# Optimization experiments

Hardware: AMD Instinct MI355X
Metric: run time of the kernel (lower is better)

Reference implementation:

```python
import jax, jax.numpy as jnp
import numpy as np

N_CHANNELS = 512
GROUPS = 8
EPS = 1e-5


def setup_inputs() -> dict:
    key = jax.random.key(0)
    ks = jax.random.split(key, 7)
    B, C, L = 8, N_CHANNELS, 4096
    s = 1.0 / np.sqrt(C)
    return {
        "x": jax.random.normal(ks[0], (B, C, L), dtype=jnp.float32),
        "gamma": jnp.ones((C,), dtype=jnp.float32),
        "beta": jnp.zeros((C,), dtype=jnp.float32),
        "w_qkv": jax.random.normal(ks[1], (3 * C, C), dtype=jnp.float32) * s,
        "b_qkv": jax.random.normal(ks[2], (3 * C,), dtype=jnp.float32) * 0.01,
        "w_out": jax.random.normal(ks[3], (C, C), dtype=jnp.float32) * s,
        "b_out": jax.random.normal(ks[4], (C,), dtype=jnp.float32) * 0.01,
    }


def group_norm(x, gamma, beta):
    # x: [B, C, L]; normalize per group of C//GROUPS channels over (channels_in_group, L)
    B, C, L = x.shape
    xg = x.reshape(B, GROUPS, C // GROUPS, L)
    mean = xg.mean(axis=(2, 3), keepdims=True)
    var = xg.var(axis=(2, 3), keepdims=True)
    xn = ((xg - mean) * jax.lax.rsqrt(var + EPS)).reshape(B, C, L)
    return xn * gamma[None, :, None] + beta[None, :, None]


def reference(x, gamma, beta, w_qkv, b_qkv, w_out, b_out):
    B, C, L = x.shape
    xn = group_norm(x, gamma, beta)
    # 1x1 conv == channel matmul: [3C, C] @ [B, C, L] -> [B, 3C, L]
    qkv = jnp.einsum('oc,bcl->bol', w_qkv, xn) + b_qkv[None, :, None]
    q, k, v = jnp.split(qkv, 3, axis=1)  # each [B, C, L]
    scale = C ** (-0.5)
    attn = jnp.einsum('bcl,bck->blk', q, k) * scale  # [B, L, L]
    attn = jax.nn.softmax(attn, axis=-1)
    out = jnp.einsum('blk,bck->bcl', attn, v)  # [B, C, L]
    proj = jnp.einsum('oc,bcl->bol', w_out, out) + b_out[None, :, None]
    return x + proj
```

## Files before the change

### kernel.cpp

```cpp
#include <hip/hip_runtime.h>

typedef __attribute__((ext_vector_type(4))) float f32x4;
typedef __attribute__((ext_vector_type(8))) short short8;
typedef unsigned short u16;
typedef unsigned int u32;

static constexpr int Bb = 8, Cc = 512, Ll = 4096;

__device__ __forceinline__ u16 f2bf(float f) {
  u32 u = __builtin_bit_cast(u32, f);
  u = (u + 0x7FFFu + ((u >> 16) & 1u)) >> 16;
  return (u16)u;
}

__device__ __forceinline__ void load_lds16(const void* g, void* l) {
  __builtin_amdgcn_global_load_lds((const __attribute__((address_space(1))) void*)g,
                                   (__attribute__((address_space(3))) void*)l,
                                   16, 0, 0);
}

__global__ void cvt_bf16_kernel(const float* __restrict__ src, u16* __restrict__ dst, int n) {
  int stride = gridDim.x * blockDim.x;
  for (int i = blockIdx.x * blockDim.x + threadIdx.x; i < n; i += stride)
    dst[i] = f2bf(src[i]);
}

__global__ __launch_bounds__(256)
void gn_stats_kernel(const float* __restrict__ x, float* __restrict__ stats) {
  int bg = blockIdx.x;
  const f32x4* p = (const f32x4*)(x + (size_t)bg * (64 * Ll));
  float s = 0.f, ss = 0.f;
  for (int i = threadIdx.x; i < 64 * Ll / 4; i += 256) {
    f32x4 v = p[i];
    s  += v[0] + v[1] + v[2] + v[3];
    ss += v[0]*v[0] + v[1]*v[1] + v[2]*v[2] + v[3]*v[3];
  }
  __shared__ float rs[256], rq[256];
  rs[threadIdx.x] = s; rq[threadIdx.x] = ss;
  __syncthreads();
  for (int st = 128; st > 0; st >>= 1) {
    if (threadIdx.x < st) { rs[threadIdx.x] += rs[threadIdx.x + st]; rq[threadIdx.x] += rq[threadIdx.x + st]; }
    __syncthreads();
  }
  if (threadIdx.x == 0) {
    const float inv_n = 1.f / (64.f * 4096.f);
    float mean = rs[0] * inv_n;
    float var  = rq[0] * inv_n - mean * mean;
    stats[bg * 2]     = mean;
    stats[bg * 2 + 1] = rsqrtf(var + 1e-5f);
  }
}

__global__ __launch_bounds__(256)
void gn_apply_t_kernel(const float* __restrict__ x, const float* __restrict__ gamma,
                       const float* __restrict__ beta, const float* __restrict__ stats,
                       u16* __restrict__ xn_t) {
  int lt = blockIdx.x;
  int ct = blockIdx.y;
  int b  = blockIdx.z;
  __shared__ float tile[64][65];
  int t = threadIdx.x;
  int lx = t & 63;
  int qd = t >> 6;
  int c0 = ct * 64, l0 = lt * 64;
  float mean = stats[(b * 8 + ct) * 2];
  float rstd = stats[(b * 8 + ct) * 2 + 1];
  #pragma unroll
  for (int i = 0; i < 16; ++i) {
    int cl = qd + i * 4;
    int c = c0 + cl;
    float v = x[((size_t)b * Cc + c) * Ll + l0 + lx];
    tile[cl][lx] = (v - mean) * rstd * gamma[c] + beta[c];
  }
  __syncthreads();
  #pragma unroll
  for (int i = 0; i < 16; ++i) {
    int ll = qd + i * 4;
    xn_t[((size_t)b * Ll + l0 + ll) * Cc + c0 + lx] = f2bf(tile[lx][ll]);
  }
}

template <int MODE>
__global__ __launch_bounds__(256, 2)
void gemm_tn(const u16* __restrict__ A, long long aStride, int lda,
             const u16* __restrict__ Bm, long long bStride, int ldb,
             void* __restrict__ Dv, long long dStride, int ldd,
             const float* __restrict__ bias, const float* __restrict__ resid, int K) {
  int z = blockIdx.z;
  A  += (size_t)z * aStride;
  Bm += (size_t)z * bStride;
  int m0 = blockIdx.x * 128, n0 = blockIdx.y * 128;
  __shared__ uint4 sA[1024], sB[1024];
  int tid = threadIdx.x, lane = tid & 63;
  int wv = tid >> 6, wr = wv >> 1, wc = wv & 1;
  int l15 = lane & 15, l4 = lane >> 4;
  f32x4 acc[4][4] = {};
  for (int kt = 0; kt < K; kt += 64) {
    __syncthreads();
    #pragma unroll
    for (int p = 0; p < 4; ++p) {
      int s = p * 256 + tid;
      int r = ((s >> 7) << 4) | (((s >> 2) & 1) << 3) | ((s >> 3) & 7);
      int g = (((s >> 6) & 1) << 2) | (s & 3);
      load_lds16(A  + (size_t)(m0 + r) * lda + kt + g * 8, &sA[s]);
      load_lds16(Bm + (size_t)(n0 + r) * ldb + kt + g * 8, &sB[s]);
    }
    __syncthreads();
    #pragma unroll
    for (int ks = 0; ks < 2; ++ks) {
      short8 af[4], bfr[4];
      #pragma unroll
      for (int i = 0; i < 4; ++i) {
        int sa = (4 * wr + i) * 128 + ks * 64 + (l15 & 7) * 8 + (l15 >> 3) * 4 + l4;
        af[i]  = *(const short8*)&sA[sa];
        int sb = (4 * wc + i) * 128 + ks * 64 + (l15 & 7) * 8 + (l15 >> 3) * 4 + l4;
        bfr[i] = *(const short8*)&sB[sb];
      }
      #pragma unroll
      for (int i = 0; i < 4; ++i)
        #pragma unroll
        for (int j = 0; j < 4; ++j)
          acc[i][j] = __builtin_amdgcn_mfma_f32_16x16x32_bf16(af[i], bfr[j], acc[i][j], 0, 0, 0);
    }
  }
  #pragma unroll
  for (int i = 0; i < 4; ++i) {
    #pragma unroll
    for (int j = 0; j < 4; ++j) {
      #pragma unroll
      for (int r = 0; r < 4; ++r) {
        int m = m0 + 64 * wr + 16 * i + 4 * l4 + r;
        int n = n0 + 64 * wc + 16 * j + l15;
        float val = acc[i][j][r] + (MODE == 0 ? bias[n] : bias[m]);
        size_t idx = (size_t)z * dStride + (size_t)m * ldd + n;
        if (MODE == 2) ((float*)Dv)[idx] = val + resid[idx];
        else           ((u16*)Dv)[idx]   = f2bf(val);
      }
    }
  }
}

__global__ __launch_bounds__(512, 2)
void flash_attn_kernel(const u16* __restrict__ qk_t, const u16* __restrict__ v,
                       u16* __restrict__ o_t) {
  int bid = blockIdx.x;
  int b  = bid & 7;
  int q0 = (bid >> 3) * 128;
  int tid = threadIdx.x, lane = tid & 63, wv = tid >> 6;
  int l15 = lane & 15, l4 = lane >> 4;
  const u16* qkb = qk_t + (size_t)b * Ll * 1024;
  const u16* vb  = v    + (size_t)b * Cc * Ll;
  u16* ob        = o_t  + (size_t)b * Ll * Cc;

  __shared__ uint4 sK[2][32 * 64];
  __shared__ uint4 sV[2][512 * 4];
  __shared__ __align__(16) char sP[128 * 64];
  __shared__ __align__(16) float sAl[128];

  int ow_q = wv >> 2, ow_c = wv & 3;

  short8 aq[16];
  {
    const u16* qp = qkb + (size_t)(q0 + wv * 16 + l15) * 1024 + 8 * l4;
    #pragma unroll
    for (int ks = 0; ks < 16; ++ks) aq[ks] = *(const short8*)(qp + 32 * ks);
  }

  auto issueK = [&](int kt, int buf) {
    #pragma unroll
    for (int p = 0; p < 4; ++p) {
      int s = p * 512 + tid;
      int kr = (((s >> 6) & 1) << 4) | (((s >> 2) & 1) << 3) | ((s >> 3) & 7);
      int g  = ((s >> 7) << 2) | (s & 3);
      load_lds16(qkb + (size_t)(kt * 32 + kr) * 1024 + 512 + g * 8, &sK[buf][s]);
    }
  };
  auto issueV = [&](int kt, int buf) {
    #pragma unroll
    for (int p = 0; p < 4; ++p) {
      int s = p * 512 + tid;
      int r = s >> 2, g = s & 3, gw = g ^ ((r >> 1) & 3);
      load_lds16(vb + (size_t)r * Ll + kt * 32 + gw * 8, &sV[buf][s]);
    }
  };
  issueK(0, 0);
  issueV(0, 0);

  f32x4 accO[4][8];
  #pragma unroll
  for (int i = 0; i < 4; ++i)
    #pragma unroll
    for (int j = 0; j < 8; ++j) accO[i][j] = (f32x4){0.f, 0.f, 0.f, 0.f};
  float mrun = -1e30f, lrun = 0.f;
  const float scale = 0.044194173824159216f;

  const int NT = Ll / 32;
  for (int kt = 0; kt < NT; ++kt) {
    int buf = kt & 1;
    __syncthreads();
    if (kt + 1 < NT) { issueK(kt + 1, buf ^ 1); issueV(kt + 1, buf ^ 1); }

    const uint4* kb = &sK[buf][0];
    f32x4 s2[2];
    #pragma unroll
    for (int t = 0; t < 2; ++t) {
      s2[t] = (f32x4){0.f, 0.f, 0.f, 0.f};
      #pragma unroll
      for (int ks = 0; ks < 16; ++ks) {
        short8 ak = *(const short8*)&kb[ks * 128 + t * 64 + (l15 & 7) * 8 + (l15 >> 3) * 4 + l4];
        s2[t] = __builtin_amdgcn_mfma_f32_16x16x32_bf16(ak, aq[ks], s2[t], 0, 0, 0);
      }
    }

    #pragma unroll
    for (int t = 0; t < 2; ++t)
      #pragma unroll
      for (int r = 0; r < 4; ++r) s2[t][r] *= scale;
    float mx = fmaxf(fmaxf(s2[0][0], s2[0][1]), fmaxf(s2[0][2], s2[0][3]));
    mx = fmaxf(mx, fmaxf(fmaxf(s2[1][0], s2[1][1]), fmaxf(s2[1][2], s2[1][3])));
    mx = fmaxf(mx, __shfl_xor(mx, 16));
    mx = fmaxf(mx, __shfl_xor(mx, 32));
    float mnew = fmaxf(mrun, mx);
    float al = __expf(mrun - mnew);
    mrun = mnew;
    float ps = 0.f;
    #pragma unroll
    for (int t = 0; t < 2; ++t)
      #pragma unroll
      for (int r = 0; r < 4; ++r) { float pv = __expf(s2[t][r] - mnew); s2[t][r] = pv; ps += pv; }
    ps += __shfl_xor(ps, 16);
    ps += __shfl_xor(ps, 32);
    lrun = lrun * al + ps;

    {
      char* pb = sP + (16 * wv + l15) * 64;
      #pragma unroll
      for (int t = 0; t < 2; ++t) {
        u32 lo = (u32)f2bf(s2[t][0]) | ((u32)f2bf(s2[t][1]) << 16);
        u32 hi = (u32)f2bf(s2[t][2]) | ((u32)f2bf(s2[t][3]) << 16);
        uint2 w = {lo, hi};
        *(uint2*)(pb + 32 * t + 8 * l4) = w;
      }
      if (lane < 16) sAl[16 * wv + lane] = al;
    }

    __builtin_amdgcn_sched_barrier(0);
    asm volatile("s_waitcnt lgkmcnt(0)" ::: "memory");
    __builtin_amdgcn_s_barrier();
    __builtin_amdgcn_sched_barrier(0);

    #pragma unroll
    for (int i = 0; i < 4; ++i) {
      f32x4 av = *(const f32x4*)&sAl[64 * ow_q + 16 * i + 4 * l4];
      #pragma unroll
      for (int j = 0; j < 8; ++j) {
        #pragma unroll
        for (int r = 0; r < 4; ++r) accO[i][j][r] *= av[r];
      }
    }
    short8 ap[4];
    #pragma unroll
    for (int i = 0; i < 4; ++i) {
      int ra = 64 * ow_q + 16 * i + l15;
      ap[i] = *(const short8*)(sP + ra * 64 + 16 * l4);
    }
    const uint4* vbuf = &sV[buf][0];
    #pragma unroll
    for (int j = 0; j < 8; ++j) {
      int crow = 128 * ow_c + 16 * j + l15;
      short8 bv = *(const short8*)&vbuf[crow * 4 + (l4 ^ ((crow >> 1) & 3))];
      #pragma unroll
      for (int i = 0; i < 4; ++i)
        accO[i][j] = __builtin_amdgcn_mfma_f32_16x16x32_bf16(ap[i], bv, accO[i][j], 0, 0, 0);
    }
  }

  __syncthreads();
  if (lane < 16) sAl[16 * wv + lane] = lrun;
  __syncthreads();
  #pragma unroll
  for (int i = 0; i < 4; ++i) {
    f32x4 lv = *(const f32x4*)&sAl[64 * ow_q + 16 * i + 4 * l4];
    #pragma unroll
    for (int r = 0; r < 4; ++r) lv[r] = 1.f / lv[r];
    #pragma unroll
    for (int j = 0; j < 8; ++j) {
      #pragma unroll
      for (int r = 0; r < 4; ++r) {
        int q = q0 + 64 * ow_q + 16 * i + 4 * l4 + r;
        int c = 128 * ow_c + 16 * j + l15;
        ob[(size_t)q * Cc + c] = f2bf(accO[i][j][r] * lv[r]);
      }
    }
  }
}

extern "C" void kernel_launch(void* const* d_in, const int* in_sizes, int n_in,
                              void* d_out, int out_size, void* d_ws, size_t ws_size,
                              hipStream_t stream) {
  const float* x     = (const float*)d_in[0];
  const float* gamma = (const float*)d_in[1];
  const float* beta  = (const float*)d_in[2];
  const float* w_qkv = (const float*)d_in[3];
  const float* b_qkv = (const float*)d_in[4];
  const float* w_out = (const float*)d_in[5];
  const float* b_out = (const float*)d_in[6];
  float* out = (float*)d_out;

  char* ws = (char*)d_ws;
  size_t off = 0;
  auto alloc = [&](size_t bytes) -> char* {
    char* p = ws + off;
    off += (bytes + 1023) & ~(size_t)1023;
    return p;
  };
  float* stats = (float*)alloc(64 * 2 * sizeof(float));
  u16* wqb = (u16*)alloc((size_t)1536 * 512 * 2);
  u16* wob = (u16*)alloc((size_t)512 * 512 * 2);
  u16* xnt = (u16*)alloc((size_t)Bb * Ll * Cc * 2);
  u16* qkt = (u16*)alloc((size_t)Bb * Ll * 1024 * 2);
  u16* vbf = (u16*)alloc((size_t)Bb * Cc * Ll * 2);
  u16* ot  = xnt;
  if (off > ws_size) return;

  cvt_bf16_kernel<<<256, 256, 0, stream>>>(w_qkv, wqb, 1536 * 512);
  cvt_bf16_kernel<<<256, 256, 0, stream>>>(w_out, wob, 512 * 512);
  gn_stats_kernel<<<64, 256, 0, stream>>>(x, stats);
  gn_apply_t_kernel<<<dim3(64, 8, 8), 256, 0, stream>>>(x, gamma, beta, stats, xnt);
  gemm_tn<0><<<dim3(32, 8, 8), 256, 0, stream>>>(
      xnt, (long long)Ll * Cc, Cc, wqb, 0, Cc,
      qkt, (long long)Ll * 1024, 1024, b_qkv, nullptr, Cc);
  gemm_tn<1><<<dim3(4, 32, 8), 256, 0, stream>>>(
      wqb + (size_t)1024 * 512, 0, Cc, xnt, (long long)Ll * Cc, Cc,
      vbf, (long long)Cc * Ll, Ll, b_qkv + 1024, nullptr, Cc);
  flash_attn_kernel<<<256, 512, 0, stream>>>(qkt, vbf, ot);
  gemm_tn<2><<<dim3(4, 32, 8), 256, 0, stream>>>(
      wob, 0, Cc, ot, (long long)Ll * Cc, Cc,
      out, (long long)Cc * Ll, Ll, b_out, x, Cc);
}
```

Measured before the change: 684.6 us.

## Software-pipeline flash attention so QK of next tile overlaps PV of previous

Restructures the attention loop so each iteration computes QK^T and softmax for tile kt while doing the rescale and PV MFMAs for tile kt-1. P and the rescale factors are double-buffered in LDS, which removes the second barrier per iteration. V loads are issued one stage later than K loads. The change also switches the K LDS layout to an XOR swizzle and pads P rows to 112 bytes to cut bank conflicts. The cost is more LDS and a more complex prologue and epilogue.

```diff
diff --git a/kernel.cpp b/kernel.cpp
--- a/kernel.cpp
+++ b/kernel.cpp
@@ -154,25 +154,17 @@
 
   __shared__ uint4 sK[2][32 * 64];
   __shared__ uint4 sV[2][512 * 4];
-  __shared__ __align__(16) char sP[128 * 64];
-  __shared__ __align__(16) float sAl[128];
+  __shared__ __align__(16) char sP[2][128 * 112];
+  __shared__ __align__(16) float sAl[2][128];
 
   int ow_q = wv >> 2, ow_c = wv & 3;
-
-  short8 aq[16];
-  {
-    const u16* qp = qkb + (size_t)(q0 + wv * 16 + l15) * 1024 + 8 * l4;
-    #pragma unroll
-    for (int ks = 0; ks < 16; ++ks) aq[ks] = *(const short8*)(qp + 32 * ks);
-  }
 
   auto issueK = [&](int kt, int buf) {
     #pragma unroll
     for (int p = 0; p < 4; ++p) {
       int s = p * 512 + tid;
-      int kr = (((s >> 6) & 1) << 4) | (((s >> 2) & 1) << 3) | ((s >> 3) & 7);
-      int g  = ((s >> 7) << 2) | (s & 3);
-      load_lds16(qkb + (size_t)(kt * 32 + kr) * 1024 + 512 + g * 8, &sK[buf][s]);
+      int r = s >> 6, g = s & 63, gw = g ^ (r & 7);
+      load_lds16(qkb + (size_t)(kt * 32 + r) * 1024 + 512 + gw * 8, &sK[buf][s]);
     }
   };
   auto issueV = [&](int kt, int buf) {
@@ -183,8 +175,15 @@
       load_lds16(vb + (size_t)r * Ll + kt * 32 + gw * 8, &sV[buf][s]);
     }
   };
+
   issueK(0, 0);
-  issueV(0, 0);
+
+  short8 aq[16];
+  {
+    const u16* qp = qkb + (size_t)(q0 + wv * 16 + l15) * 1024 + 8 * l4;
+    #pragma unroll
+    for (int ks = 0; ks < 16; ++ks) aq[ks] = *(const short8*)(qp + 32 * ks);
+  }
 
   f32x4 accO[4][8];
   #pragma unroll
@@ -193,25 +192,22 @@
     for (int j = 0; j < 8; ++j) accO[i][j] = (f32x4){0.f, 0.f, 0.f, 0.f};
   float mrun = -1e30f, lrun = 0.f;
   const float scale = 0.044194173824159216f;
-
   const int NT = Ll / 32;
-  for (int kt = 0; kt < NT; ++kt) {
-    int buf = kt & 1;
-    __syncthreads();
-    if (kt + 1 < NT) { issueK(kt + 1, buf ^ 1); issueV(kt + 1, buf ^ 1); }
-
+
+  auto qk_compute = [&](int buf, f32x4* s2) {
     const uint4* kb = &sK[buf][0];
-    f32x4 s2[2];
     #pragma unroll
     for (int t = 0; t < 2; ++t) {
       s2[t] = (f32x4){0.f, 0.f, 0.f, 0.f};
+      int krow = 16 * t + l15;
       #pragma unroll
       for (int ks = 0; ks < 16; ++ks) {
-        short8 ak = *(const short8*)&kb[ks * 128 + t * 64 + (l15 & 7) * 8 + (l15 >> 3) * 4 + l4];
+        short8 ak = *(const short8*)&kb[krow * 64 + ((4 * ks + l4) ^ (krow & 7))];
         s2[t] = __builtin_amdgcn_mfma_f32_16x16x32_bf16(ak, aq[ks], s2[t], 0, 0, 0);
       }
     }
-
+  };
+  auto softmax_store = [&](int buf, f32x4* s2) {
     #pragma unroll
     for (int t = 0; t < 2; ++t)
       #pragma unroll
@@ -231,27 +227,20 @@
     ps += __shfl_xor(ps, 16);
     ps += __shfl_xor(ps, 32);
     lrun = lrun * al + ps;
-
-    {
-      char* pb = sP + (16 * wv + l15) * 64;
-      #pragma unroll
-      for (int t = 0; t < 2; ++t) {
-        u32 lo = (u32)f2bf(s2[t][0]) | ((u32)f2bf(s2[t][1]) << 16);
-        u32 hi = (u32)f2bf(s2[t][2]) | ((u32)f2bf(s2[t][3]) << 16);
-        uint2 w = {lo, hi};
-        *(uint2*)(pb + 32 * t + 8 * l4) = w;
-      }
-      if (lane < 16) sAl[16 * wv + lane] = al;
-    }
-
-    __builtin_amdgcn_sched_barrier(0);
-    asm volatile("s_waitcnt lgkmcnt(0)" ::: "memory");
-    __builtin_amdgcn_s_barrier();
-    __builtin_amdgcn_sched_barrier(0);
-
+    char* pb = &sP[buf][0] + (16 * wv + l15) * 112;
+    #pragma unroll
+    for (int t = 0; t < 2; ++t) {
+      u32 lo = (u32)f2bf(s2[t][0]) | ((u32)f2bf(s2[t][1]) << 16);
+      u32 hi = (u32)f2bf(s2[t][2]) | ((u32)f2bf(s2[t][3]) << 16);
+      uint2 w = {lo, hi};
+      *(uint2*)(pb + 32 * t + 8 * l4) = w;
+    }
+    if (lane < 16) sAl[buf][16 * wv + lane] = al;
+  };
+  auto rescale_pv = [&](int pb) {
     #pragma unroll
     for (int i = 0; i < 4; ++i) {
-      f32x4 av = *(const f32x4*)&sAl[64 * ow_q + 16 * i + 4 * l4];
+      f32x4 av = *(const f32x4*)&sAl[pb][64 * ow_q + 16 * i + 4 * l4];
       #pragma unroll
       for (int j = 0; j < 8; ++j) {
         #pragma unroll
@@ -262,9 +251,9 @@
     #pragma unroll
     for (int i = 0; i < 4; ++i) {
       int ra = 64 * ow_q + 16 * i + l15;
-      ap[i] = *(const short8*)(sP + ra * 64 + 16 * l4);
-    }
-    const uint4* vbuf = &sV[buf][0];
+      ap[i] = *(const short8*)(&sP[pb][0] + ra * 112 + 16 * l4);
+    }
+    const uint4* vbuf = &sV[pb][0];
     #pragma unroll
     for (int j = 0; j < 8; ++j) {
       int crow = 128 * ow_c + 16 * j + l15;
@@ -273,14 +262,35 @@
       for (int i = 0; i < 4; ++i)
         accO[i][j] = __builtin_amdgcn_mfma_f32_16x16x32_bf16(ap[i], bv, accO[i][j], 0, 0, 0);
     }
-  }
-
-  __syncthreads();
-  if (lane < 16) sAl[16 * wv + lane] = lrun;
+  };
+
+  __syncthreads();
+  issueK(1, 1);
+  issueV(0, 0);
+  {
+    f32x4 s2[2];
+    qk_compute(0, s2);
+    softmax_store(0, s2);
+  }
+
+  for (int kt = 1; kt < NT; ++kt) {
+    int buf = kt & 1;
+    __syncthreads();
+    if (kt + 1 < NT) issueK(kt + 1, buf ^ 1);
+    issueV(kt, buf);
+    f32x4 s2[2];
+    qk_compute(buf, s2);
+    rescale_pv(buf ^ 1);
+    softmax_store(buf, s2);
+  }
+
+  __syncthreads();
+  rescale_pv((NT - 1) & 1);
+  if (lane < 16) sAl[NT & 1][16 * wv + lane] = lrun;
   __syncthreads();
   #pragma unroll
   for (int i = 0; i < 4; ++i) {
-    f32x4 lv = *(const f32x4*)&sAl[64 * ow_q + 16 * i + 4 * l4];
+    f32x4 lv = *(const f32x4*)&sAl[NT & 1][64 * ow_q + 16 * i + 4 * l4];
     #pragma unroll
     for (int r = 0; r < 4; ++r) lv[r] = 1.f / lv[r];
     #pragma unroll
```

After: 736.6 us. 7.6% more time.

## Shrink attention blocks to 64 queries with single-buffered swizzled K/V tiles

Applied to the files above, without the earlier changes.

The flash attention kernel now uses 256-thread blocks handling 64 queries each, doubling the grid to 512 blocks. The K/V double-buffer prefetch is replaced by a single buffer loaded each iteration, with a partial vmcnt wait so the QK product can start once K has arrived while V is still loading. K tiles use a row-XOR swizzle and the P buffer rows are padded to reduce LDS bank conflicts. This aims to improve occupancy and load balance, but it doubles K/V global traffic per query and exposes load latency that was previously hidden by prefetching.

```diff
diff --git a/kernel.cpp b/kernel.cpp
--- a/kernel.cpp
+++ b/kernel.cpp
@@ -140,24 +140,22 @@
   }
 }
 
-__global__ __launch_bounds__(512, 2)
+__global__ __launch_bounds__(256, 2)
 void flash_attn_kernel(const u16* __restrict__ qk_t, const u16* __restrict__ v,
                        u16* __restrict__ o_t) {
   int bid = blockIdx.x;
   int b  = bid & 7;
-  int q0 = (bid >> 3) * 128;
+  int q0 = (bid >> 3) * 64;
   int tid = threadIdx.x, lane = tid & 63, wv = tid >> 6;
   int l15 = lane & 15, l4 = lane >> 4;
   const u16* qkb = qk_t + (size_t)b * Ll * 1024;
   const u16* vb  = v    + (size_t)b * Cc * Ll;
   u16* ob        = o_t  + (size_t)b * Ll * Cc;
 
-  __shared__ uint4 sK[2][32 * 64];
-  __shared__ uint4 sV[2][512 * 4];
-  __shared__ __align__(16) char sP[128 * 64];
-  __shared__ __align__(16) float sAl[128];
-
-  int ow_q = wv >> 2, ow_c = wv & 3;
+  __shared__ uint4 sK[32 * 64];
+  __shared__ uint4 sV[512 * 4];
+  __shared__ __align__(16) char sP[64 * 80];
+  __shared__ __align__(16) float sAl[64];
 
   short8 aq[16];
   {
@@ -166,25 +164,22 @@
     for (int ks = 0; ks < 16; ++ks) aq[ks] = *(const short8*)(qp + 32 * ks);
   }
 
-  auto issueK = [&](int kt, int buf) {
-    #pragma unroll
-    for (int p = 0; p < 4; ++p) {
-      int s = p * 512 + tid;
-      int kr = (((s >> 6) & 1) << 4) | (((s >> 2) & 1) << 3) | ((s >> 3) & 7);
-      int g  = ((s >> 7) << 2) | (s & 3);
-      load_lds16(qkb + (size_t)(kt * 32 + kr) * 1024 + 512 + g * 8, &sK[buf][s]);
+  auto issueK = [&](int kt) {
+    #pragma unroll
+    for (int p = 0; p < 8; ++p) {
+      int s = p * 256 + tid;
+      int r = s >> 6, g = s & 63, gw = g ^ (r & 7);
+      load_lds16(qkb + (size_t)(kt * 32 + r) * 1024 + 512 + gw * 8, &sK[s]);
     }
   };
-  auto issueV = [&](int kt, int buf) {
-    #pragma unroll
-    for (int p = 0; p < 4; ++p) {
-      int s = p * 512 + tid;
+  auto issueV = [&](int kt) {
+    #pragma unroll
+    for (int p = 0; p < 8; ++p) {
+      int s = p * 256 + tid;
       int r = s >> 2, g = s & 3, gw = g ^ ((r >> 1) & 3);
-      load_lds16(vb + (size_t)r * Ll + kt * 32 + gw * 8, &sV[buf][s]);
+      load_lds16(vb + (size_t)r * Ll + kt * 32 + gw * 8, &sV[s]);
     }
   };
-  issueK(0, 0);
-  issueV(0, 0);
 
   f32x4 accO[4][8];
   #pragma unroll
@@ -196,18 +191,21 @@
 
   const int NT = Ll / 32;
   for (int kt = 0; kt < NT; ++kt) {
-    int buf = kt & 1;
     __syncthreads();
-    if (kt + 1 < NT) { issueK(kt + 1, buf ^ 1); issueV(kt + 1, buf ^ 1); }
-
-    const uint4* kb = &sK[buf][0];
+    issueK(kt);
+    issueV(kt);
+    asm volatile("s_waitcnt vmcnt(8)" ::: "memory");
+    __builtin_amdgcn_s_barrier();
+    __builtin_amdgcn_sched_barrier(0);
+
     f32x4 s2[2];
     #pragma unroll
     for (int t = 0; t < 2; ++t) {
       s2[t] = (f32x4){0.f, 0.f, 0.f, 0.f};
+      int krow = 16 * t + l15;
       #pragma unroll
       for (int ks = 0; ks < 16; ++ks) {
-        short8 ak = *(const short8*)&kb[ks * 128 + t * 64 + (l15 & 7) * 8 + (l15 >> 3) * 4 + l4];
+        short8 ak = *(const short8*)&sK[krow * 64 + ((4 * ks + l4) ^ (krow & 7))];
         s2[t] = __builtin_amdgcn_mfma_f32_16x16x32_bf16(ak, aq[ks], s2[t], 0, 0, 0);
       }
     }
@@ -233,7 +231,7 @@
     lrun = lrun * al + ps;
 
     {
-      char* pb = sP + (16 * wv + l15) * 64;
+      char* pb = sP + (16 * wv + l15) * 80;
       #pragma unroll
       for (int t = 0; t < 2; ++t) {
         u32 lo = (u32)f2bf(s2[t][0]) | ((u32)f2bf(s2[t][1]) << 16);
@@ -245,13 +243,13 @@
     }
 
     __builtin_amdgcn_sched_barrier(0);
-    asm volatile("s_waitcnt lgkmcnt(0)" ::: "memory");
+    asm volatile("s_waitcnt vmcnt(0) lgkmcnt(0)" ::: "memory");
     __builtin_amdgcn_s_barrier();
     __builtin_amdgcn_sched_barrier(0);
 
     #pragma unroll
     for (int i = 0; i < 4; ++i) {
-      f32x4 av = *(const f32x4*)&sAl[64 * ow_q + 16 * i + 4 * l4];
+      f32x4 av = *(const f32x4*)&sAl[16 * i + 4 * l4];
       #pragma unroll
       for (int j = 0; j < 8; ++j) {
         #pragma unroll
@@ -261,14 +259,13 @@
     short8 ap[4];
     #pragma unroll
     for (int i = 0; i < 4; ++i) {
-      int ra = 64 * ow_q + 16 * i + l15;
-      ap[i] = *(const short8*)(sP + ra * 64 + 16 * l4);
-    }
-    const uint4* vbuf = &sV[buf][0];
+      int ra = 16 * i + l15;
+      ap[i] = *(const short8*)(sP + ra * 80 + 16 * l4);
+    }
     #pragma unroll
     for (int j = 0; j < 8; ++j) {
-      int crow = 128 * ow_c + 16 * j + l15;
-      short8 bv = *(const short8*)&vbuf[crow * 4 + (l4 ^ ((crow >> 1) & 3))];
+      int crow = 128 * wv + 16 * j + l15;
+      short8 bv = *(const short8*)&sV[crow * 4 + (l4 ^ ((crow >> 1) & 3))];
       #pragma unroll
       for (int i = 0; i < 4; ++i)
         accO[i][j] = __builtin_amdgcn_mfma_f32_16x16x32_bf16(ap[i], bv, accO[i][j], 0, 0, 0);
@@ -280,15 +277,15 @@
   __syncthreads();
   #pragma unroll
   for (int i = 0; i < 4; ++i) {
-    f32x4 lv = *(const f32x4*)&sAl[64 * ow_q + 16 * i + 4 * l4];
+    f32x4 lv = *(const f32x4*)&sAl[16 * i + 4 * l4];
     #pragma unroll
     for (int r = 0; r < 4; ++r) lv[r] = 1.f / lv[r];
     #pragma unroll
     for (int j = 0; j < 8; ++j) {
       #pragma unroll
       for (int r = 0; r < 4; ++r) {
-        int q = q0 + 64 * ow_q + 16 * i + 4 * l4 + r;
-        int c = 128 * ow_c + 16 * j + l15;
+        int q = q0 + 16 * i + 4 * l4 + r;
+        int c = 128 * wv + 16 * j + l15;
         ob[(size_t)q * Cc + c] = f2bf(accO[i][j][r] * lv[r]);
       }
     }
@@ -333,7 +330,7 @@
   gemm_tn<1><<<dim3(4, 32, 8), 256, 0, stream>>>(
       wqb + (size_t)1024 * 512, 0, Cc, xnt, (long long)Ll * Cc, Cc,
       vbf, (long long)Cc * Ll, Ll, b_qkv + 1024, nullptr, Cc);
-  flash_attn_kernel<<<256, 512, 0, stream>>>(qkt, vbf, ot);
+  flash_attn_kernel<<<512, 256, 0, stream>>>(qkt, vbf, ot);
   gemm_tn<2><<<dim3(4, 32, 8), 256, 0, stream>>>(
       wob, 0, Cc, ot, (long long)Ll * Cc, Cc,
       out, (long long)Cc * Ll, Ll, b_out, x, Cc);
```

New measurement: 841.0 us. +22.8%, slower.

## Use 64-key tiles with single-buffered K/V and staggered async loads

Applied to the files above, without the earlier changes.

Doubles the key tile per iteration from 32 to 64 and halves the loop trip count. K and V move from double-buffered LDS to single buffers with an XOR swizzle. The next K tile is issued once the QK^T phase is done, and the next V tile after the PV phase, with vmcnt waits in between. The aim is fewer barriers and softmax-rescale passes per key, keeping LDS use near 150KB for two blocks per CU, but load latency is now overlapped with only half of each iteration's compute.

```diff
diff --git a/kernel.cpp b/kernel.cpp
--- a/kernel.cpp
+++ b/kernel.cpp
@@ -152,9 +152,9 @@
   const u16* vb  = v    + (size_t)b * Cc * Ll;
   u16* ob        = o_t  + (size_t)b * Ll * Cc;
 
-  __shared__ uint4 sK[2][32 * 64];
-  __shared__ uint4 sV[2][512 * 4];
-  __shared__ __align__(16) char sP[128 * 64];
+  __shared__ uint4 sK[64 * 64];
+  __shared__ uint4 sV[512 * 8];
+  __shared__ __align__(16) char sP[128 * 144];
   __shared__ __align__(16) float sAl[128];
 
   int ow_q = wv >> 2, ow_c = wv & 3;
@@ -166,25 +166,24 @@
     for (int ks = 0; ks < 16; ++ks) aq[ks] = *(const short8*)(qp + 32 * ks);
   }
 
-  auto issueK = [&](int kt, int buf) {
-    #pragma unroll
-    for (int p = 0; p < 4; ++p) {
+  auto issueK = [&](int kt) {
+    #pragma unroll
+    for (int p = 0; p < 8; ++p) {
       int s = p * 512 + tid;
-      int kr = (((s >> 6) & 1) << 4) | (((s >> 2) & 1) << 3) | ((s >> 3) & 7);
-      int g  = ((s >> 7) << 2) | (s & 3);
-      load_lds16(qkb + (size_t)(kt * 32 + kr) * 1024 + 512 + g * 8, &sK[buf][s]);
+      int r = s >> 6, g = s & 63, gw = g ^ (r & 7);
+      load_lds16(qkb + (size_t)(kt * 64 + r) * 1024 + 512 + gw * 8, &sK[s]);
     }
   };
-  auto issueV = [&](int kt, int buf) {
-    #pragma unroll
-    for (int p = 0; p < 4; ++p) {
+  auto issueV = [&](int kt) {
+    #pragma unroll
+    for (int p = 0; p < 8; ++p) {
       int s = p * 512 + tid;
-      int r = s >> 2, g = s & 3, gw = g ^ ((r >> 1) & 3);
-      load_lds16(vb + (size_t)r * Ll + kt * 32 + gw * 8, &sV[buf][s]);
+      int r = s >> 3, g = s & 7, gw = g ^ (r & 7);
+      load_lds16(vb + (size_t)r * Ll + kt * 64 + gw * 8, &sV[s]);
     }
   };
-  issueK(0, 0);
-  issueV(0, 0);
+  issueK(0);
+  issueV(0);
 
   f32x4 accO[4][8];
   #pragma unroll
@@ -194,30 +193,33 @@
   float mrun = -1e30f, lrun = 0.f;
   const float scale = 0.044194173824159216f;
 
-  const int NT = Ll / 32;
+  const int NT = Ll / 64;
   for (int kt = 0; kt < NT; ++kt) {
-    int buf = kt & 1;
-    __syncthreads();
-    if (kt + 1 < NT) { issueK(kt + 1, buf ^ 1); issueV(kt + 1, buf ^ 1); }
-
-    const uint4* kb = &sK[buf][0];
-    f32x4 s2[2];
-    #pragma unroll
-    for (int t = 0; t < 2; ++t) {
+    asm volatile("s_waitcnt vmcnt(8)" ::: "memory");
+    __builtin_amdgcn_s_barrier();
+    __builtin_amdgcn_sched_barrier(0);
+
+    f32x4 s2[4];
+    #pragma unroll
+    for (int t = 0; t < 4; ++t) {
       s2[t] = (f32x4){0.f, 0.f, 0.f, 0.f};
+      int krow = 16 * t + l15;
       #pragma unroll
       for (int ks = 0; ks < 16; ++ks) {
-        short8 ak = *(const short8*)&kb[ks * 128 + t * 64 + (l15 & 7) * 8 + (l15 >> 3) * 4 + l4];
+        short8 ak = *(const short8*)&sK[krow * 64 + ((4 * ks + l4) ^ (krow & 7))];
         s2[t] = __builtin_amdgcn_mfma_f32_16x16x32_bf16(ak, aq[ks], s2[t], 0, 0, 0);
       }
     }
 
     #pragma unroll
-    for (int t = 0; t < 2; ++t)
+    for (int t = 0; t < 4; ++t)
       #pragma unroll
       for (int r = 0; r < 4; ++r) s2[t][r] *= scale;
-    float mx = fmaxf(fmaxf(s2[0][0], s2[0][1]), fmaxf(s2[0][2], s2[0][3]));
-    mx = fmaxf(mx, fmaxf(fmaxf(s2[1][0], s2[1][1]), fmaxf(s2[1][2], s2[1][3])));
+    float mx = -1e30f;
+    #pragma unroll
+    for (int t = 0; t < 4; ++t)
+      #pragma unroll
+      for (int r = 0; r < 4; ++r) mx = fmaxf(mx, s2[t][r]);
     mx = fmaxf(mx, __shfl_xor(mx, 16));
     mx = fmaxf(mx, __shfl_xor(mx, 32));
     float mnew = fmaxf(mrun, mx);
@@ -225,7 +227,7 @@
     mrun = mnew;
     float ps = 0.f;
     #pragma unroll
-    for (int t = 0; t < 2; ++t)
+    for (int t = 0; t < 4; ++t)
       #pragma unroll
       for (int r = 0; r < 4; ++r) { float pv = __expf(s2[t][r] - mnew); s2[t][r] = pv; ps += pv; }
     ps += __shfl_xor(ps, 16);
@@ -233,9 +235,9 @@
     lrun = lrun * al + ps;
 
     {
-      char* pb = sP + (16 * wv + l15) * 64;
-      #pragma unroll
-      for (int t = 0; t < 2; ++t) {
+      char* pb = sP + (16 * wv + l15) * 144;
+      #pragma unroll
+      for (int t = 0; t < 4; ++t) {
         u32 lo = (u32)f2bf(s2[t][0]) | ((u32)f2bf(s2[t][1]) << 16);
         u32 hi = (u32)f2bf(s2[t][2]) | ((u32)f2bf(s2[t][3]) << 16);
         uint2 w = {lo, hi};
@@ -245,9 +247,10 @@
     }
 
     __builtin_amdgcn_sched_barrier(0);
-    asm volatile("s_waitcnt lgkmcnt(0)" ::: "memory");
+    asm volatile("s_waitcnt vmcnt(0) lgkmcnt(0)" ::: "memory");
     __builtin_amdgcn_s_barrier();
     __builtin_amdgcn_sched_barrier(0);
+    if (kt + 1 < NT) issueK(kt + 1);
 
     #pragma unroll
     for (int i = 0; i < 4; ++i) {
@@ -258,24 +261,31 @@
         for (int r = 0; r < 4; ++r) accO[i][j][r] *= av[r];
       }
     }
-    short8 ap[4];
-    #pragma unroll
-    for (int i = 0; i < 4; ++i) {
-      int ra = 64 * ow_q + 16 * i + l15;
-      ap[i] = *(const short8*)(sP + ra * 64 + 16 * l4);
-    }
-    const uint4* vbuf = &sV[buf][0];
-    #pragma unroll
-    for (int j = 0; j < 8; ++j) {
-      int crow = 128 * ow_c + 16 * j + l15;
-      short8 bv = *(const short8*)&vbuf[crow * 4 + (l4 ^ ((crow >> 1) & 3))];
-      #pragma unroll
-      for (int i = 0; i < 4; ++i)
-        accO[i][j] = __builtin_amdgcn_mfma_f32_16x16x32_bf16(ap[i], bv, accO[i][j], 0, 0, 0);
-    }
-  }
-
-  __syncthreads();
+    #pragma unroll
+    for (int ks = 0; ks < 2; ++ks) {
+      short8 ap[4];
+      #pragma unroll
+      for (int i = 0; i < 4; ++i) {
+        int ra = 64 * ow_q + 16 * i + l15;
+        ap[i] = *(const short8*)(sP + ra * 144 + 64 * ks + 16 * l4);
+      }
+      #pragma unroll
+      for (int j = 0; j < 8; ++j) {
+        int crow = 128 * ow_c + 16 * j + l15;
+        short8 bv = *(const short8*)&sV[crow * 8 + ((4 * ks + l4) ^ (crow & 7))];
+        #pragma unroll
+        for (int i = 0; i < 4; ++i)
+          accO[i][j] = __builtin_amdgcn_mfma_f32_16x16x32_bf16(ap[i], bv, accO[i][j], 0, 0, 0);
+      }
+    }
+
+    __builtin_amdgcn_sched_barrier(0);
+    asm volatile("s_waitcnt lgkmcnt(0)" ::: "memory");
+    __builtin_amdgcn_s_barrier();
+    __builtin_amdgcn_sched_barrier(0);
+    if (kt + 1 < NT) issueV(kt + 1);
+  }
+
   if (lane < 16) sAl[16 * wv + lane] = lrun;
   __syncthreads();
   #pragma unroll
```

Measured after the change: 1.131 ms. 65.2% more time.
